# Performance work log

Measured on AMD Instinct MI355X. Metric: run time of the kernel, lower is better.

Reference implementation:

```python
import jax, jax.numpy as jnp
import numpy as np


def setup_inputs() -> dict:
    key = jax.random.key(0)
    k1, k2 = jax.random.split(key)
    b, s, h = 32, 4096, 1024
    decoder_state_t = jax.random.normal(k1, (b, h), dtype=jnp.float32)
    encoder_outputs = jax.random.normal(k2, (b, s, h), dtype=jnp.float32)
    return {"decoder_state_t": decoder_state_t, "encoder_outputs": encoder_outputs}


def reference(decoder_state_t, encoder_outputs):
    # scores[b,s] = sum_h decoder_state_t[b,h] * encoder_outputs[b,s,h]
    scores = jnp.einsum("bh,bsh->bs", decoder_state_t, encoder_outputs)
    attn = jax.nn.softmax(scores, axis=-1)
    # context[b,h] = sum_s attn[b,s] * encoder_outputs[b,s,h]
    context = jnp.einsum("bs,bsh->bh", attn, encoder_outputs)
    return (context, attn)
```

## Files before the change

### kernel.cpp

```cpp
#include <hip/hip_runtime.h>
#include <math.h>

#define B 32
#define S 4096
#define H 1024
#define NCHUNK 32
#define ROWS_PER_BLOCK (S / NCHUNK)
#define ROWS_PER_WAVE (ROWS_PER_BLOCK/4)
#define PSTRIDE 1040

__device__ __forceinline__ float dot4(float4 a, float4 b) {
    return fmaf(a.x, b.x, fmaf(a.y, b.y, fmaf(a.z, b.z, a.w * b.w)));
}

__global__ __launch_bounds__(256) void attn_pass1(
    const float* __restrict__ dec, const float* __restrict__ enc,
    float* __restrict__ scores, float* __restrict__ part)
{
    const int blk   = blockIdx.x;
    const int b     = blk / NCHUNK;
    const int chunk = blk % NCHUNK;
    const int lane  = threadIdx.x & 63;
    const int w     = threadIdx.x >> 6;

    const float4* dsp = (const float4*)(dec + (size_t)b * H);
    float4 dsv[4];
#pragma unroll
    for (int q = 0; q < 4; ++q) dsv[q] = dsp[q * 64 + lane];

    float m = -INFINITY, l = 0.f;
    float4 accq[4];
#pragma unroll
    for (int q = 0; q < 4; ++q) accq[q] = make_float4(0.f, 0.f, 0.f, 0.f);

    const int row0 = chunk * ROWS_PER_BLOCK + w * ROWS_PER_WAVE;
    const float4* base = (const float4*)(enc + ((size_t)b * S + row0) * H);

    float4 buf[2][2][4];
#pragma unroll
    for (int q = 0; q < 4; ++q) {
        buf[0][0][q] = base[q * 64 + lane];
        buf[0][1][q] = base[256 + q * 64 + lane];
    }

#pragma unroll
    for (int rr = 0; rr < ROWS_PER_WAVE; rr += 2) {
        const int pc = (rr >> 1) & 1;
        const int pn = pc ^ 1;
        if (rr + 2 < ROWS_PER_WAVE) {
            const float4* nb = base + (size_t)(rr + 2) * 256;
#pragma unroll
            for (int q = 0; q < 4; ++q) {
                buf[pn][0][q] = nb[q * 64 + lane];
                buf[pn][1][q] = nb[256 + q * 64 + lane];
            }
        }

        float s0 = (dot4(buf[pc][0][0], dsv[0]) + dot4(buf[pc][0][1], dsv[1]))
                 + (dot4(buf[pc][0][2], dsv[2]) + dot4(buf[pc][0][3], dsv[3]));
        float s1 = (dot4(buf[pc][1][0], dsv[0]) + dot4(buf[pc][1][1], dsv[1]))
                 + (dot4(buf[pc][1][2], dsv[2]) + dot4(buf[pc][1][3], dsv[3]));

#pragma unroll
        for (int d = 32; d >= 1; d >>= 1) {
            s0 += __shfl_xor(s0, d);
            s1 += __shfl_xor(s1, d);
        }

        if (lane == 0) {
            float2 sv = make_float2(s0, s1);
            *(float2*)&scores[(size_t)b * S + row0 + rr] = sv;
        }

        const float mn = fmaxf(m, fmaxf(s0, s1));
        const float a  = __expf(m - mn);
        const float p0 = __expf(s0 - mn);
        const float p1 = __expf(s1 - mn);
        m = mn;
        l = fmaf(l, a, p0 + p1);
#pragma unroll
        for (int q = 0; q < 4; ++q) {
            const float4 e0 = buf[pc][0][q];
            const float4 e1 = buf[pc][1][q];
            accq[q].x = fmaf(p1, e1.x, fmaf(p0, e0.x, accq[q].x * a));
            accq[q].y = fmaf(p1, e1.y, fmaf(p0, e0.y, accq[q].y * a));
            accq[q].z = fmaf(p1, e1.z, fmaf(p0, e0.z, accq[q].z * a));
            accq[q].w = fmaf(p1, e1.w, fmaf(p0, e0.w, accq[q].w * a));
        }
    }

    __shared__ float sm[4], sl[4];
    __shared__ float sc[4][1024];
    if (lane == 0) { sm[w] = m; sl[w] = l; }
#pragma unroll
    for (int q = 0; q < 4; ++q)
        *(float4*)&sc[w][(q * 64 + lane) * 4] = accq[q];
    __syncthreads();

    const float M  = fmaxf(fmaxf(sm[0], sm[1]), fmaxf(sm[2], sm[3]));
    const float al0 = __expf(sm[0] - M), al1 = __expf(sm[1] - M);
    const float al2 = __expf(sm[2] - M), al3 = __expf(sm[3] - M);
    const float Lb = sl[0]*al0 + sl[1]*al1 + sl[2]*al2 + sl[3]*al3;

    const int t = threadIdx.x;
    const float4 c0 = *(const float4*)&sc[0][t * 4];
    const float4 c1 = *(const float4*)&sc[1][t * 4];
    const float4 c2 = *(const float4*)&sc[2][t * 4];
    const float4 c3 = *(const float4*)&sc[3][t * 4];
    float4 cp;
    cp.x = c0.x*al0 + c1.x*al1 + c2.x*al2 + c3.x*al3;
    cp.y = c0.y*al0 + c1.y*al1 + c2.y*al2 + c3.y*al3;
    cp.z = c0.z*al0 + c1.z*al1 + c2.z*al2 + c3.z*al3;
    cp.w = c0.w*al0 + c1.w*al1 + c2.w*al2 + c3.w*al3;

    float* pb = part + (size_t)blk * PSTRIDE;
    *(float4*)&pb[t * 4] = cp;
    if (t == 0) { pb[1024] = M; pb[1025] = Lb; }
}

__global__ __launch_bounds__(256) void attn_pass2(
    const float* __restrict__ scores, const float* __restrict__ part,
    float* __restrict__ out)
{
    const int b = blockIdx.x >> 2;
    const int j = blockIdx.x & 3;
    const int t = threadIdx.x;
    const float* pbase = part + (size_t)b * NCHUNK * PSTRIDE;

    float M = -INFINITY;
    for (int i = 0; i < NCHUNK; ++i)
        M = fmaxf(M, pbase[i * PSTRIDE + 1024]);
    float L = 0.f;
    for (int i = 0; i < NCHUNK; ++i)
        L += pbase[i * PSTRIDE + 1025] * __expf(pbase[i * PSTRIDE + 1024] - M);
    const float invL = 1.f / L;

    const int h = j * 256 + t;
    float acc = 0.f;
    for (int i = 0; i < NCHUNK; ++i)
        acc = fmaf(__expf(pbase[i * PSTRIDE + 1024] - M),
                   pbase[i * PSTRIDE + h], acc);
    out[(size_t)b * H + h] = acc * invL;

    float* attn_out = out + (size_t)B * H;
    for (int k = 0; k < 4; ++k) {
        const int s = j * 1024 + k * 256 + t;
        attn_out[(size_t)b * S + s] =
            __expf(scores[(size_t)b * S + s] - M) * invL;
    }
}

extern "C" void kernel_launch(void* const* d_in, const int* in_sizes, int n_in,
                              void* d_out, int out_size, void* d_ws, size_t ws_size,
                              hipStream_t stream) {
    const float* dec = (const float*)d_in[0];
    const float* enc = (const float*)d_in[1];
    float* out = (float*)d_out;
    float* ws  = (float*)d_ws;
    float* scores = ws;
    float* part   = ws + (size_t)B * S;

    attn_pass1<<<B * NCHUNK, 256, 0, stream>>>(dec, enc, scores, part);
    attn_pass2<<<B * 4, 256, 0, stream>>>(scores, part, out);
}
```

Measured before the change: 757.7 us.

## Use nontemporal single-row loads and write per-wave partials instead of block reduction

Pass 1 now processes one encoder row per iteration with a single-row prefetch, using nontemporal loads (the encoder data is streamed once), and no longer fully unrolls the row loop. The in-block shared-memory merge and __syncthreads are removed; each wave writes its own partial context, max and sum, so pass 2 reduces four times as many partials per batch. This cuts registers and LDS use and the block barrier, in exchange for less memory-level parallelism per wave and more partial traffic in pass 2.

```diff
diff --git a/kernel.cpp b/kernel.cpp
--- a/kernel.cpp
+++ b/kernel.cpp
@@ -6,10 +6,14 @@
 #define H 1024
 #define NCHUNK 32
 #define ROWS_PER_BLOCK (S / NCHUNK)
-#define ROWS_PER_WAVE (ROWS_PER_BLOCK/4)
+#define ROWS_PER_WAVE  (ROWS_PER_BLOCK/4)
+#define PPB 4
+#define NPART_PER_B (NCHUNK * PPB)
 #define PSTRIDE 1040
 
-__device__ __forceinline__ float dot4(float4 a, float4 b) {
+typedef float v4 __attribute__((ext_vector_type(4)));
+
+__device__ __forceinline__ float dot4v(v4 a, v4 b) {
     return fmaf(a.x, b.x, fmaf(a.y, b.y, fmaf(a.z, b.z, a.w * b.w)));
 }
 
@@ -23,99 +27,60 @@
     const int lane  = threadIdx.x & 63;
     const int w     = threadIdx.x >> 6;
 
-    const float4* dsp = (const float4*)(dec + (size_t)b * H);
-    float4 dsv[4];
+    const v4* dsp = (const v4*)(dec + (size_t)b * H);
+    v4 dsv[4];
 #pragma unroll
     for (int q = 0; q < 4; ++q) dsv[q] = dsp[q * 64 + lane];
 
     float m = -INFINITY, l = 0.f;
-    float4 accq[4];
+    v4 accq[4];
 #pragma unroll
-    for (int q = 0; q < 4; ++q) accq[q] = make_float4(0.f, 0.f, 0.f, 0.f);
+    for (int q = 0; q < 4; ++q) accq[q] = (v4)(0.f);
 
     const int row0 = chunk * ROWS_PER_BLOCK + w * ROWS_PER_WAVE;
-    const float4* base = (const float4*)(enc + ((size_t)b * S + row0) * H);
+    const v4* base = (const v4*)(enc + ((size_t)b * S + row0) * H);
+    float* srow = scores + (size_t)b * S + row0;
 
-    float4 buf[2][2][4];
+    v4 cur[4], nxt[4];
 #pragma unroll
-    for (int q = 0; q < 4; ++q) {
-        buf[0][0][q] = base[q * 64 + lane];
-        buf[0][1][q] = base[256 + q * 64 + lane];
-    }
+    for (int q = 0; q < 4; ++q)
+        cur[q] = __builtin_nontemporal_load(&base[q * 64 + lane]);
 
+#pragma unroll 1
+    for (int r = 0; r < ROWS_PER_WAVE; ++r) {
+        if (r + 1 < ROWS_PER_WAVE) {
+            const v4* nb = base + (size_t)(r + 1) * (H / 4);
 #pragma unroll
-    for (int rr = 0; rr < ROWS_PER_WAVE; rr += 2) {
-        const int pc = (rr >> 1) & 1;
-        const int pn = pc ^ 1;
-        if (rr + 2 < ROWS_PER_WAVE) {
-            const float4* nb = base + (size_t)(rr + 2) * 256;
-#pragma unroll
-            for (int q = 0; q < 4; ++q) {
-                buf[pn][0][q] = nb[q * 64 + lane];
-                buf[pn][1][q] = nb[256 + q * 64 + lane];
-            }
+            for (int q = 0; q < 4; ++q)
+                nxt[q] = __builtin_nontemporal_load(&nb[q * 64 + lane]);
         }
 
-        float s0 = (dot4(buf[pc][0][0], dsv[0]) + dot4(buf[pc][0][1], dsv[1]))
-                 + (dot4(buf[pc][0][2], dsv[2]) + dot4(buf[pc][0][3], dsv[3]));
-        float s1 = (dot4(buf[pc][1][0], dsv[0]) + dot4(buf[pc][1][1], dsv[1]))
-                 + (dot4(buf[pc][1][2], dsv[2]) + dot4(buf[pc][1][3], dsv[3]));
+        float s = (dot4v(cur[0], dsv[0]) + dot4v(cur[1], dsv[1]))
+                + (dot4v(cur[2], dsv[2]) + dot4v(cur[3], dsv[3]));
+#pragma unroll
+        for (int d = 32; d >= 1; d >>= 1) s += __shfl_xor(s, d);
+        if (lane == 0) srow[r] = s;
 
-#pragma unroll
-        for (int d = 32; d >= 1; d >>= 1) {
-            s0 += __shfl_xor(s0, d);
-            s1 += __shfl_xor(s1, d);
-        }
-
-        if (lane == 0) {
-            float2 sv = make_float2(s0, s1);
-            *(float2*)&scores[(size_t)b * S + row0 + rr] = sv;
-        }
-
-        const float mn = fmaxf(m, fmaxf(s0, s1));
+        const float mn = fmaxf(m, s);
         const float a  = __expf(m - mn);
-        const float p0 = __expf(s0 - mn);
-        const float p1 = __expf(s1 - mn);
+        const float p  = __expf(s - mn);
         m = mn;
-        l = fmaf(l, a, p0 + p1);
+        l = fmaf(l, a, p);
 #pragma unroll
         for (int q = 0; q < 4; ++q) {
-            const float4 e0 = buf[pc][0][q];
-            const float4 e1 = buf[pc][1][q];
-            accq[q].x = fmaf(p1, e1.x, fmaf(p0, e0.x, accq[q].x * a));
-            accq[q].y = fmaf(p1, e1.y, fmaf(p0, e0.y, accq[q].y * a));
-            accq[q].z = fmaf(p1, e1.z, fmaf(p0, e0.z, accq[q].z * a));
-            accq[q].w = fmaf(p1, e1.w, fmaf(p0, e0.w, accq[q].w * a));
+            accq[q].x = fmaf(p, cur[q].x, accq[q].x * a);
+            accq[q].y = fmaf(p, cur[q].y, accq[q].y * a);
+            accq[q].z = fmaf(p, cur[q].z, accq[q].z * a);
+            accq[q].w = fmaf(p, cur[q].w, accq[q].w * a);
+            cur[q] = nxt[q];
         }
     }
 
-    __shared__ float sm[4], sl[4];
-    __shared__ float sc[4][1024];
-    if (lane == 0) { sm[w] = m; sl[w] = l; }
+    float* pb = part + ((size_t)blk * PPB + w) * PSTRIDE;
 #pragma unroll
     for (int q = 0; q < 4; ++q)
-        *(float4*)&sc[w][(q * 64 + lane) * 4] = accq[q];
-    __syncthreads();
-
-    const float M  = fmaxf(fmaxf(sm[0], sm[1]), fmaxf(sm[2], sm[3]));
-    const float al0 = __expf(sm[0] - M), al1 = __expf(sm[1] - M);
-    const float al2 = __expf(sm[2] - M), al3 = __expf(sm[3] - M);
-    const float Lb = sl[0]*al0 + sl[1]*al1 + sl[2]*al2 + sl[3]*al3;
-
-    const int t = threadIdx.x;
-    const float4 c0 = *(const float4*)&sc[0][t * 4];
-    const float4 c1 = *(const float4*)&sc[1][t * 4];
-    const float4 c2 = *(const float4*)&sc[2][t * 4];
-    const float4 c3 = *(const float4*)&sc[3][t * 4];
-    float4 cp;
-    cp.x = c0.x*al0 + c1.x*al1 + c2.x*al2 + c3.x*al3;
-    cp.y = c0.y*al0 + c1.y*al1 + c2.y*al2 + c3.y*al3;
-    cp.z = c0.z*al0 + c1.z*al1 + c2.z*al2 + c3.z*al3;
-    cp.w = c0.w*al0 + c1.w*al1 + c2.w*al2 + c3.w*al3;
-
-    float* pb = part + (size_t)blk * PSTRIDE;
-    *(float4*)&pb[t * 4] = cp;
-    if (t == 0) { pb[1024] = M; pb[1025] = Lb; }
+        *(v4*)&pb[(q * 64 + lane) * 4] = accq[q];
+    if (lane == 0) { pb[1024] = m; pb[1025] = l; }
 }
 
 __global__ __launch_bounds__(256) void attn_pass2(
@@ -125,19 +90,19 @@
     const int b = blockIdx.x >> 2;
     const int j = blockIdx.x & 3;
     const int t = threadIdx.x;
-    const float* pbase = part + (size_t)b * NCHUNK * PSTRIDE;
+    const float* pbase = part + (size_t)b * NPART_PER_B * PSTRIDE;
 
     float M = -INFINITY;
-    for (int i = 0; i < NCHUNK; ++i)
+    for (int i = 0; i < NPART_PER_B; ++i)
         M = fmaxf(M, pbase[i * PSTRIDE + 1024]);
     float L = 0.f;
-    for (int i = 0; i < NCHUNK; ++i)
+    for (int i = 0; i < NPART_PER_B; ++i)
         L += pbase[i * PSTRIDE + 1025] * __expf(pbase[i * PSTRIDE + 1024] - M);
     const float invL = 1.f / L;
 
     const int h = j * 256 + t;
     float acc = 0.f;
-    for (int i = 0; i < NCHUNK; ++i)
+    for (int i = 0; i < NPART_PER_B; ++i)
         acc = fmaf(__expf(pbase[i * PSTRIDE + 1024] - M),
                    pbase[i * PSTRIDE + h], acc);
     out[(size_t)b * H + h] = acc * invL;
```

Result: faster. 690.1 us (-8.9%).
